# Kernel optimization log

Hardware: AMD Instinct MI355X
Metric: run time of the kernel (lower is better)

Reference implementation:

```python
import jax, jax.numpy as jnp
import numpy as np

N_NODES = 100000
N_EDGES = 3200000
IN_DIM = 256
EMB_DIM = 64
BATCH = 4096
WEIGHT_DECAY = 1e-4


def setup_inputs() -> dict:
    key = jax.random.key(0)
    ks = jax.random.split(key, 8)
    feats = jax.random.normal(ks[0], (N_NODES, IN_DIM), dtype=jnp.float32)
    W = jax.random.normal(ks[1], (IN_DIM, EMB_DIM), dtype=jnp.float32) * (1.0 / np.sqrt(IN_DIM))
    edge_row = jax.random.randint(ks[2], (N_EDGES,), 0, N_NODES, dtype=jnp.int32)
    edge_col = jax.random.randint(ks[3], (N_EDGES,), 0, N_NODES, dtype=jnp.int32)
    edge_val = jax.random.uniform(ks[4], (N_EDGES,), dtype=jnp.float32) * 0.05  # normalized adj weights
    idx1 = jax.random.randint(ks[5], (BATCH,), 0, N_NODES, dtype=jnp.int32)
    idx2 = jax.random.randint(ks[6], (BATCH,), 0, N_NODES, dtype=jnp.int32)
    neg_idx = jax.random.randint(ks[7], (BATCH,), 0, N_NODES, dtype=jnp.int32)
    return {"feats": feats, "W": W, "edge_row": edge_row, "edge_col": edge_col,
            "edge_val": edge_val, "idx1": idx1, "idx2": idx2, "neg_idx": neg_idx}


def reference(feats, W, edge_row, edge_col, edge_val, idx1, idx2, neg_idx):
    # GraphConvolution: tanh( A_sparse @ (X @ W) ), A in COO form
    xw = feats @ W                                              # [N, D]
    msgs = edge_val[:, None] * xw[edge_col]                     # [E, D] gather + scale
    h = jax.ops.segment_sum(msgs, edge_row, num_segments=N_NODES)  # sparse-dense matmul
    h = jnp.tanh(h)
    # tf.nn.l2_normalize(embedding, 1)
    sq = jnp.sum(h * h, axis=1, keepdims=True)
    emb = h * jax.lax.rsqrt(jnp.maximum(sq, 1e-12))             # [N, D]
    # embedding lookups
    o1, o2, on = emb[idx1], emb[idx2], emb[neg_idx]             # [B, D] each
    y_ui = jnp.sum(o1 * o2, axis=1)
    y_uj = jnp.sum(o1 * on, axis=1)
    # BPR loss + weight decay (tf.nn.l2_loss = 0.5*sum(x^2))
    bpr = jnp.sum(-jax.nn.log_sigmoid(y_ui - y_uj))
    loss = (bpr + WEIGHT_DECAY * 0.5 * jnp.sum(emb * emb)) / jnp.float32(BATCH)
    return loss
```

## Files before the change

kernel.cpp:

```cpp
#include <hip/hip_runtime.h>
#include <cmath>

#define N_NODES 100000
#define N_EDGES 3200000
#define IN_DIM 256
#define EMB 64
#define BATCH 4096
#define MWAVES 6250
#define NBUCK 782
#define BROWS 128
#define BSTRIDE 4608
#define EPB 4096

typedef unsigned long long u64;
typedef unsigned int u32;
typedef unsigned short u16;
typedef __attribute__((ext_vector_type(8))) short bf16x8;
typedef __attribute__((ext_vector_type(4))) float f32x4;

__device__ __forceinline__ float wave_sum(float v) {
#pragma unroll
    for (int m = 1; m < 64; m <<= 1) v += __shfl_xor(v, m, 64);
    return v;
}

__device__ __forceinline__ u16 f2bf_rne(float f) {
    u32 u = __float_as_uint(f);
    u32 r = ((u >> 16) & 1u) + 0x7FFFu;
    return (u16)((u + r) >> 16);
}

__device__ __forceinline__ float bf2f(u32 bits16) {
    return __uint_as_float(bits16 << 16);
}

__global__ __launch_bounds__(256) void mfma_gemm_kernel(const float* __restrict__ feats,
                                                        const float* __restrict__ W,
                                                        u16* __restrict__ xwb) {
    __shared__ u16 wlds[32 * 64 * 8];
    const int tid = threadIdx.x;
    for (int idx = tid; idx < 32 * 64; idx += 256) {
        const int f = idx >> 6, lane = idx & 63;
        const int kt = f >> 2, nt = f & 3;
        const int k0 = kt * 32 + (lane >> 4) * 8;
        const int n  = nt * 16 + (lane & 15);
        u32 buf[4];
#pragma unroll
        for (int jj = 0; jj < 4; ++jj) {
            u16 lo = f2bf_rne(W[(size_t)(k0 + 2 * jj) * EMB + n]);
            u16 hi = f2bf_rne(W[(size_t)(k0 + 2 * jj + 1) * EMB + n]);
            buf[jj] = (u32)lo | ((u32)hi << 16);
        }
        *(uint4*)&wlds[idx * 8] = *(uint4*)buf;
    }
    __syncthreads();

    const int wave = tid >> 6, lane = tid & 63;
    const int wid = blockIdx.x * 4 + wave;
    if (wid >= MWAVES) return;
    const int row0 = wid * 16;
    const int arow = row0 + (lane & 15);
    const int kbase = (lane >> 4) * 8;
    const float* fr = feats + (size_t)arow * IN_DIM + kbase;

    float4 av[16];
#pragma unroll
    for (int kt = 0; kt < 8; ++kt) {
        av[2 * kt]     = *(const float4*)(fr + kt * 32);
        av[2 * kt + 1] = *(const float4*)(fr + kt * 32 + 4);
    }

    f32x4 acc[4] = {};
    const u16* wl = &wlds[lane * 8];
#pragma unroll
    for (int kt = 0; kt < 8; ++kt) {
        float4 a0 = av[2 * kt], a1 = av[2 * kt + 1];
        u32 ab[4];
        ab[0] = (u32)f2bf_rne(a0.x) | ((u32)f2bf_rne(a0.y) << 16);
        ab[1] = (u32)f2bf_rne(a0.z) | ((u32)f2bf_rne(a0.w) << 16);
        ab[2] = (u32)f2bf_rne(a1.x) | ((u32)f2bf_rne(a1.y) << 16);
        ab[3] = (u32)f2bf_rne(a1.z) | ((u32)f2bf_rne(a1.w) << 16);
        bf16x8 afrag = *(bf16x8*)ab;
#pragma unroll
        for (int nt = 0; nt < 4; ++nt) {
            bf16x8 bfrag = *(const bf16x8*)&wl[(kt * 4 + nt) * 512];
            acc[nt] = __builtin_amdgcn_mfma_f32_16x16x32_bf16(afrag, bfrag, acc[nt], 0, 0, 0);
        }
    }
    const int rb = row0 + (lane >> 4) * 4;
    const int cb = lane & 15;
#pragma unroll
    for (int nt = 0; nt < 4; ++nt)
#pragma unroll
        for (int r = 0; r < 4; ++r)
            xwb[(size_t)(rb + r) * EMB + nt * 16 + cb] = f2bf_rne(acc[nt][r]);
}

__global__ __launch_bounds__(256) void passA_kernel(const int* __restrict__ erow,
                                                    const int* __restrict__ ecol,
                                                    const float* __restrict__ eval,
                                                    u32* __restrict__ gcursor,
                                                    u64* __restrict__ sorted) {
    __shared__ u64 stage[EPB];
    __shared__ u32 hist[1024];
    __shared__ u32 offs[1024];
    __shared__ u32 cursor[1024];
    __shared__ u32 gbase[1024];
    __shared__ u32 partial[256];

    const int tid = threadIdx.x;
    const int e0 = blockIdx.x * EPB;
    const int total = min(EPB, N_EDGES - e0);

    for (int i = tid; i < 1024; i += 256) hist[i] = 0;
    __syncthreads();

    u64 ent[16];
    int eb[16];
#pragma unroll
    for (int j = 0; j < 16; ++j) {
        const int e = e0 + j * 256 + tid;
        if (e < N_EDGES) {
            const int r = erow[e];
            const int c = ecol[e];
            const u16 vb = f2bf_rne(eval[e]);
            ent[j] = (u64)(u32)r | ((u64)(u32)c << 17) | ((u64)vb << 34);
            eb[j] = r >> 7;
            atomicAdd(&hist[eb[j]], 1u);
        } else {
            eb[j] = -1;
        }
    }
    __syncthreads();

    u32 local[4], s = 0;
#pragma unroll
    for (int q = 0; q < 4; ++q) {
        local[q] = s;
        s += hist[4 * tid + q];
    }
    partial[tid] = s;
    __syncthreads();
    for (int off = 1; off < 256; off <<= 1) {
        u32 x = (tid >= off) ? partial[tid - off] : 0;
        __syncthreads();
        partial[tid] += x;
        __syncthreads();
    }
    const u32 base = partial[tid] - s;
#pragma unroll
    for (int q = 0; q < 4; ++q) {
        offs[4 * tid + q] = base + local[q];
        cursor[4 * tid + q] = base + local[q];
    }
    __syncthreads();

#pragma unroll
    for (int j = 0; j < 16; ++j) {
        if (eb[j] >= 0) {
            u32 pos = atomicAdd(&cursor[eb[j]], 1u);
            stage[pos] = ent[j];
        }
    }
    __syncthreads();

    for (int b = tid; b < 1024; b += 256) {
        const u32 cnt = cursor[b] - offs[b];
        gbase[b] = cnt ? atomicAdd(&gcursor[b], cnt) : 0;
    }
    __syncthreads();

    for (int i = tid; i < total; i += 256) {
        const u64 p = stage[i];
        const int b = (int)(p & 0x1FFFFu) >> 7;
        const u32 gpos = gbase[b] + ((u32)i - offs[b]);
        if (gpos < BSTRIDE) sorted[(size_t)b * BSTRIDE + gpos] = p;
    }
}

__global__ __launch_bounds__(1024, 8) void gather_kernel(const u16* __restrict__ xwb,
                                                         u64* __restrict__ sorted,
                                                         const u32* __restrict__ gcursor,
                                                         float* __restrict__ accumA) {
    __shared__ u64 stage[BSTRIDE];
    __shared__ u32 rhist[BROWS], roff[BROWS], rcur[BROWS], sc[BROWS];
    __shared__ float part[16];
    const int tid = threadIdx.x, wave = tid >> 6, lane = tid & 63;
    const int b = blockIdx.x;
    u64* gbase = sorted + (size_t)b * BSTRIDE;
    const int cnt = min((int)gcursor[b], BSTRIDE);

    if (tid < BROWS) rhist[tid] = 0;
    __syncthreads();

    u64 ent[5];
    int nloc = 0;
    for (int i = tid; i < cnt; i += 1024) {
        u64 p = gbase[i];
        ent[nloc++] = p;
        atomicAdd(&rhist[(int)(p & 127u)], 1u);
    }
    __syncthreads();

    if (tid < BROWS) sc[tid] = rhist[tid];
    __syncthreads();
    for (int off = 1; off < BROWS; off <<= 1) {
        u32 x = (tid < BROWS && tid >= off) ? sc[tid - off] : 0;
        __syncthreads();
        if (tid < BROWS) sc[tid] += x;
        __syncthreads();
    }
    if (tid < BROWS) {
        roff[tid] = sc[tid] - rhist[tid];
        rcur[tid] = sc[tid] - rhist[tid];
    }
    __syncthreads();

    for (int j = 0; j < nloc; ++j) {
        const u64 p = ent[j];
        const u32 pos = atomicAdd(&rcur[(int)(p & 127u)], 1u);
        stage[pos] = p;
    }
    __syncthreads();

    u16* embp = (u16*)gbase;
    float wd = 0.f;
    for (int rr = 0; rr < 8; ++rr) {
        const int r = wave * 8 + rr;
        const int s0 = roff[r], n = rhist[r];
        float acc = 0.f;
        int j = s0;
        const int e2 = s0 + n;
        for (; j + 7 < e2; j += 8) {
            u64 p0 = stage[j],     p1 = stage[j + 1], p2 = stage[j + 2], p3 = stage[j + 3];
            u64 p4 = stage[j + 4], p5 = stage[j + 5], p6 = stage[j + 6], p7 = stage[j + 7];
            float x0 = bf2f(xwb[(size_t)((p0 >> 17) & 0x1FFFFu) * EMB + lane]);
            float x1 = bf2f(xwb[(size_t)((p1 >> 17) & 0x1FFFFu) * EMB + lane]);
            float x2 = bf2f(xwb[(size_t)((p2 >> 17) & 0x1FFFFu) * EMB + lane]);
            float x3 = bf2f(xwb[(size_t)((p3 >> 17) & 0x1FFFFu) * EMB + lane]);
            float x4 = bf2f(xwb[(size_t)((p4 >> 17) & 0x1FFFFu) * EMB + lane]);
            float x5 = bf2f(xwb[(size_t)((p5 >> 17) & 0x1FFFFu) * EMB + lane]);
            float x6 = bf2f(xwb[(size_t)((p6 >> 17) & 0x1FFFFu) * EMB + lane]);
            float x7 = bf2f(xwb[(size_t)((p7 >> 17) & 0x1FFFFu) * EMB + lane]);
            acc += bf2f((u32)(p0 >> 34) & 0xFFFFu) * x0 + bf2f((u32)(p1 >> 34) & 0xFFFFu) * x1;
            acc += bf2f((u32)(p2 >> 34) & 0xFFFFu) * x2 + bf2f((u32)(p3 >> 34) & 0xFFFFu) * x3;
            acc += bf2f((u32)(p4 >> 34) & 0xFFFFu) * x4 + bf2f((u32)(p5 >> 34) & 0xFFFFu) * x5;
            acc += bf2f((u32)(p6 >> 34) & 0xFFFFu) * x6 + bf2f((u32)(p7 >> 34) & 0xFFFFu) * x7;
        }
        for (; j < e2; ++j) {
            u64 p = stage[j];
            acc += bf2f((u32)(p >> 34) & 0xFFFFu) * bf2f(xwb[(size_t)((p >> 17) & 0x1FFFFu) * EMB + lane]);
        }
        float x = tanhf(acc);
        float sq = wave_sum(x * x);
        if (b * BROWS + r < N_NODES)
            embp[r * EMB + lane] = f2bf_rne(x * rsqrtf(fmaxf(sq, 1e-12f)));
        wd += sq / fmaxf(sq, 1e-12f);
    }
    if (lane == 0) part[wave] = wd;
    __syncthreads();
    if (tid == 0) {
        float v = 0.f;
#pragma unroll
        for (int w = 0; w < 16; ++w) v += part[w];
        unsafeAtomicAdd(&accumA[b & 255], v);
    }
}

__device__ __forceinline__ float emb_ld(const u64* __restrict__ sorted, int row, int lane) {
    const u16* rp = (const u16*)(sorted + (size_t)(row >> 7) * BSTRIDE) + (row & 127) * EMB;
    return bf2f(rp[lane]);
}

__global__ __launch_bounds__(256) void bpr_kernel(const u64* __restrict__ sorted,
                                                  const int* __restrict__ idx1,
                                                  const int* __restrict__ idx2,
                                                  const int* __restrict__ nidx,
                                                  float* __restrict__ accumB) {
    const int wave = threadIdx.x >> 6, lane = threadIdx.x & 63;
    const int i = blockIdx.x * 4 + wave;
    float o1 = emb_ld(sorted, idx1[i], lane);
    float o2 = emb_ld(sorted, idx2[i], lane);
    float on = emb_ld(sorted, nidx[i], lane);
    float yui = wave_sum(o1 * o2);
    float yuj = wave_sum(o1 * on);
    if (lane == 0) {
        float x = yui - yuj;
        float li = (x > 0.f) ? log1pf(expf(-x)) : (-x + log1pf(expf(x)));
        unsafeAtomicAdd(&accumB[i & 255], li);
    }
}

__global__ __launch_bounds__(64) void finalize_kernel(const float* __restrict__ accumA,
                                                      const float* __restrict__ accumB,
                                                      float* __restrict__ out) {
    const int t = threadIdx.x;
    float wd = 0.f, bp = 0.f;
#pragma unroll
    for (int k = 0; k < 4; ++k) {
        wd += accumA[t + 64 * k];
        bp += accumB[t + 64 * k];
    }
    wd = wave_sum(wd);
    bp = wave_sum(bp);
    if (t == 0) out[0] = (bp + 1e-4f * 0.5f * wd) / (float)BATCH;
}

extern "C" void kernel_launch(void* const* d_in, const int* in_sizes, int n_in,
                              void* d_out, int out_size, void* d_ws, size_t ws_size,
                              hipStream_t stream) {
    const float* feats = (const float*)d_in[0];
    const float* W     = (const float*)d_in[1];
    const int*   erow  = (const int*)d_in[2];
    const int*   ecol  = (const int*)d_in[3];
    const float* eval  = (const float*)d_in[4];
    const int*   idx1  = (const int*)d_in[5];
    const int*   idx2  = (const int*)d_in[6];
    const int*   nidx  = (const int*)d_in[7];
    float* out = (float*)d_out;

    u16*   xwb     = (u16*)d_ws;
    u64*   sorted  = (u64*)(xwb + (size_t)N_NODES * EMB);
    u32*   gcursor = (u32*)(sorted + (size_t)NBUCK * BSTRIDE);
    float* accumA  = (float*)(gcursor + 1024);
    float* accumB  = accumA + 256;

    hipMemsetAsync(gcursor, 0, (1024 + 512) * sizeof(u32), stream);

    mfma_gemm_kernel<<<(MWAVES + 3) / 4, 256, 0, stream>>>(feats, W, xwb);
    passA_kernel<<<(N_EDGES + EPB - 1) / EPB, 256, 0, stream>>>(erow, ecol, eval, gcursor, sorted);
    gather_kernel<<<NBUCK, 1024, 0, stream>>>(xwb, sorted, gcursor, accumA);
    bpr_kernel<<<BATCH / 4, 256, 0, stream>>>(sorted, idx1, idx2, nidx, accumB);
    finalize_kernel<<<1, 64, 0, stream>>>(accumA, accumB, out);
}
```

Baseline: 345.3 us.

## Fuse GEMM and edge bucketing into one kernel, fold finalize into BPR

Merges the bf16 MFMA projection GEMM and the edge-bucketing pass into a single launch with interleaved block types, so the compute-bound GEMM and the memory-bound scatter can run at the same time. Block size moves to 512 and the GEMM loads its A operand in two halves to cut register pressure. Gather blocks shrink to 512 threads, each wave now handling 16 rows. The finalize kernel is removed: the last BPR block, found with an atomic counter, does the final reduction, which saves a launch but adds a threadfence and an atomic per block.

```diff
diff --git a/kernel.cpp b/kernel.cpp
--- a/kernel.cpp
+++ b/kernel.cpp
@@ -11,6 +11,8 @@
 #define BROWS 128
 #define BSTRIDE 4608
 #define EPB 4096
+#define GSUB 782
+#define ASUB 782
 
 typedef unsigned long long u64;
 typedef unsigned int u32;
@@ -34,157 +36,157 @@
     return __uint_as_float(bits16 << 16);
 }
 
-__global__ __launch_bounds__(256) void mfma_gemm_kernel(const float* __restrict__ feats,
-                                                        const float* __restrict__ W,
-                                                        u16* __restrict__ xwb) {
-    __shared__ u16 wlds[32 * 64 * 8];
+__global__ __launch_bounds__(512, 6) void fused_kernel(const float* __restrict__ feats,
+                                                       const float* __restrict__ W,
+                                                       u16* __restrict__ xwb,
+                                                       const int* __restrict__ erow,
+                                                       const int* __restrict__ ecol,
+                                                       const float* __restrict__ eval,
+                                                       u32* __restrict__ gcursor,
+                                                       u64* __restrict__ sorted) {
+    __shared__ u64 smem[5376];
     const int tid = threadIdx.x;
-    for (int idx = tid; idx < 32 * 64; idx += 256) {
-        const int f = idx >> 6, lane = idx & 63;
-        const int kt = f >> 2, nt = f & 3;
-        const int k0 = kt * 32 + (lane >> 4) * 8;
-        const int n  = nt * 16 + (lane & 15);
-        u32 buf[4];
-#pragma unroll
-        for (int jj = 0; jj < 4; ++jj) {
-            u16 lo = f2bf_rne(W[(size_t)(k0 + 2 * jj) * EMB + n]);
-            u16 hi = f2bf_rne(W[(size_t)(k0 + 2 * jj + 1) * EMB + n]);
-            buf[jj] = (u32)lo | ((u32)hi << 16);
-        }
-        *(uint4*)&wlds[idx * 8] = *(uint4*)buf;
-    }
-    __syncthreads();
-
-    const int wave = tid >> 6, lane = tid & 63;
-    const int wid = blockIdx.x * 4 + wave;
-    if (wid >= MWAVES) return;
-    const int row0 = wid * 16;
-    const int arow = row0 + (lane & 15);
-    const int kbase = (lane >> 4) * 8;
-    const float* fr = feats + (size_t)arow * IN_DIM + kbase;
-
-    float4 av[16];
-#pragma unroll
-    for (int kt = 0; kt < 8; ++kt) {
-        av[2 * kt]     = *(const float4*)(fr + kt * 32);
-        av[2 * kt + 1] = *(const float4*)(fr + kt * 32 + 4);
-    }
-
-    f32x4 acc[4] = {};
-    const u16* wl = &wlds[lane * 8];
-#pragma unroll
-    for (int kt = 0; kt < 8; ++kt) {
-        float4 a0 = av[2 * kt], a1 = av[2 * kt + 1];
-        u32 ab[4];
-        ab[0] = (u32)f2bf_rne(a0.x) | ((u32)f2bf_rne(a0.y) << 16);
-        ab[1] = (u32)f2bf_rne(a0.z) | ((u32)f2bf_rne(a0.w) << 16);
-        ab[2] = (u32)f2bf_rne(a1.x) | ((u32)f2bf_rne(a1.y) << 16);
-        ab[3] = (u32)f2bf_rne(a1.z) | ((u32)f2bf_rne(a1.w) << 16);
-        bf16x8 afrag = *(bf16x8*)ab;
-#pragma unroll
-        for (int nt = 0; nt < 4; ++nt) {
-            bf16x8 bfrag = *(const bf16x8*)&wl[(kt * 4 + nt) * 512];
-            acc[nt] = __builtin_amdgcn_mfma_f32_16x16x32_bf16(afrag, bfrag, acc[nt], 0, 0, 0);
-        }
-    }
-    const int rb = row0 + (lane >> 4) * 4;
-    const int cb = lane & 15;
-#pragma unroll
-    for (int nt = 0; nt < 4; ++nt)
-#pragma unroll
-        for (int r = 0; r < 4; ++r)
-            xwb[(size_t)(rb + r) * EMB + nt * 16 + cb] = f2bf_rne(acc[nt][r]);
-}
-
-__global__ __launch_bounds__(256) void passA_kernel(const int* __restrict__ erow,
-                                                    const int* __restrict__ ecol,
-                                                    const float* __restrict__ eval,
-                                                    u32* __restrict__ gcursor,
-                                                    u64* __restrict__ sorted) {
-    __shared__ u64 stage[EPB];
-    __shared__ u32 hist[1024];
-    __shared__ u32 offs[1024];
-    __shared__ u32 cursor[1024];
-    __shared__ u32 gbase[1024];
-    __shared__ u32 partial[256];
-
-    const int tid = threadIdx.x;
-    const int e0 = blockIdx.x * EPB;
-    const int total = min(EPB, N_EDGES - e0);
-
-    for (int i = tid; i < 1024; i += 256) hist[i] = 0;
-    __syncthreads();
-
-    u64 ent[16];
-    int eb[16];
-#pragma unroll
-    for (int j = 0; j < 16; ++j) {
-        const int e = e0 + j * 256 + tid;
-        if (e < N_EDGES) {
-            const int r = erow[e];
-            const int c = ecol[e];
-            const u16 vb = f2bf_rne(eval[e]);
-            ent[j] = (u64)(u32)r | ((u64)(u32)c << 17) | ((u64)vb << 34);
-            eb[j] = r >> 7;
-            atomicAdd(&hist[eb[j]], 1u);
-        } else {
-            eb[j] = -1;
-        }
-    }
-    __syncthreads();
-
-    u32 local[4], s = 0;
-#pragma unroll
-    for (int q = 0; q < 4; ++q) {
-        local[q] = s;
-        s += hist[4 * tid + q];
-    }
-    partial[tid] = s;
-    __syncthreads();
-    for (int off = 1; off < 256; off <<= 1) {
-        u32 x = (tid >= off) ? partial[tid - off] : 0;
-        __syncthreads();
-        partial[tid] += x;
-        __syncthreads();
-    }
-    const u32 base = partial[tid] - s;
-#pragma unroll
-    for (int q = 0; q < 4; ++q) {
-        offs[4 * tid + q] = base + local[q];
-        cursor[4 * tid + q] = base + local[q];
-    }
-    __syncthreads();
-
-#pragma unroll
-    for (int j = 0; j < 16; ++j) {
-        if (eb[j] >= 0) {
-            u32 pos = atomicAdd(&cursor[eb[j]], 1u);
-            stage[pos] = ent[j];
-        }
-    }
-    __syncthreads();
-
-    for (int b = tid; b < 1024; b += 256) {
-        const u32 cnt = cursor[b] - offs[b];
-        gbase[b] = cnt ? atomicAdd(&gcursor[b], cnt) : 0;
-    }
-    __syncthreads();
-
-    for (int i = tid; i < total; i += 256) {
-        const u64 p = stage[i];
-        const int b = (int)(p & 0x1FFFFu) >> 7;
-        const u32 gpos = gbase[b] + ((u32)i - offs[b]);
-        if (gpos < BSTRIDE) sorted[(size_t)b * BSTRIDE + gpos] = p;
-    }
-}
-
-__global__ __launch_bounds__(1024, 8) void gather_kernel(const u16* __restrict__ xwb,
-                                                         u64* __restrict__ sorted,
-                                                         const u32* __restrict__ gcursor,
-                                                         float* __restrict__ accumA) {
+    const int type = blockIdx.x & 1;
+    const int sub = blockIdx.x >> 1;
+
+    if (type == 0) {
+        u16* wlds = (u16*)smem;
+        for (int idx = tid; idx < 32 * 64; idx += 512) {
+            const int f = idx >> 6, lane = idx & 63;
+            const int kt = f >> 2, nt = f & 3;
+            const int k0 = kt * 32 + (lane >> 4) * 8;
+            const int n  = nt * 16 + (lane & 15);
+            u32 buf[4];
+#pragma unroll
+            for (int jj = 0; jj < 4; ++jj) {
+                u16 lo = f2bf_rne(W[(size_t)(k0 + 2 * jj) * EMB + n]);
+                u16 hi = f2bf_rne(W[(size_t)(k0 + 2 * jj + 1) * EMB + n]);
+                buf[jj] = (u32)lo | ((u32)hi << 16);
+            }
+            *(uint4*)&wlds[idx * 8] = *(uint4*)buf;
+        }
+        __syncthreads();
+
+        const int wave = tid >> 6, lane = tid & 63;
+        const int wid = sub * 8 + wave;
+        if (wid >= MWAVES) return;
+        const int row0 = wid * 16;
+        const int arow = row0 + (lane & 15);
+        const int kbase = (lane >> 4) * 8;
+        const float* fr = feats + (size_t)arow * IN_DIM + kbase;
+
+        f32x4 acc[4] = {};
+        const u16* wl = &wlds[lane * 8];
+#pragma unroll
+        for (int half = 0; half < 2; ++half) {
+            float4 av[8];
+#pragma unroll
+            for (int k2 = 0; k2 < 4; ++k2) {
+                const int kt = half * 4 + k2;
+                av[2 * k2]     = *(const float4*)(fr + kt * 32);
+                av[2 * k2 + 1] = *(const float4*)(fr + kt * 32 + 4);
+            }
+#pragma unroll
+            for (int k2 = 0; k2 < 4; ++k2) {
+                const int kt = half * 4 + k2;
+                float4 a0 = av[2 * k2], a1 = av[2 * k2 + 1];
+                u32 ab[4];
+                ab[0] = (u32)f2bf_rne(a0.x) | ((u32)f2bf_rne(a0.y) << 16);
+                ab[1] = (u32)f2bf_rne(a0.z) | ((u32)f2bf_rne(a0.w) << 16);
+                ab[2] = (u32)f2bf_rne(a1.x) | ((u32)f2bf_rne(a1.y) << 16);
+                ab[3] = (u32)f2bf_rne(a1.z) | ((u32)f2bf_rne(a1.w) << 16);
+                bf16x8 afrag = *(bf16x8*)ab;
+#pragma unroll
+                for (int nt = 0; nt < 4; ++nt) {
+                    bf16x8 bfrag = *(const bf16x8*)&wl[(kt * 4 + nt) * 512];
+                    acc[nt] = __builtin_amdgcn_mfma_f32_16x16x32_bf16(afrag, bfrag, acc[nt], 0, 0, 0);
+                }
+            }
+        }
+        const int rb = row0 + (lane >> 4) * 4;
+        const int cb = lane & 15;
+#pragma unroll
+        for (int nt = 0; nt < 4; ++nt)
+#pragma unroll
+            for (int r = 0; r < 4; ++r)
+                xwb[(size_t)(rb + r) * EMB + nt * 16 + cb] = f2bf_rne(acc[nt][r]);
+    } else {
+        u64* stage    = smem;
+        u32* histoffs = (u32*)(smem + 4096);
+        u32* cursor   = (u32*)(smem + 4608);
+        u32* partial  = (u32*)(smem + 5120);
+
+        const int e0 = sub * EPB;
+        const int total = min(EPB, N_EDGES - e0);
+
+        for (int i = tid; i < 1024; i += 512) histoffs[i] = 0;
+        __syncthreads();
+
+        u64 ent[8];
+        int eb[8];
+#pragma unroll
+        for (int j = 0; j < 8; ++j) {
+            const int e = e0 + j * 512 + tid;
+            if (e < N_EDGES) {
+                const int r = erow[e];
+                const int c = ecol[e];
+                const u16 vb = f2bf_rne(eval[e]);
+                ent[j] = (u64)(u32)r | ((u64)(u32)c << 17) | ((u64)vb << 34);
+                eb[j] = r >> 7;
+                atomicAdd(&histoffs[eb[j]], 1u);
+            } else {
+                eb[j] = -1;
+            }
+        }
+        __syncthreads();
+
+        const u32 c0 = histoffs[2 * tid], c1 = histoffs[2 * tid + 1];
+        const u32 s = c0 + c1;
+        partial[tid] = s;
+        __syncthreads();
+        for (int off = 1; off < 512; off <<= 1) {
+            u32 x = (tid >= off) ? partial[tid - off] : 0;
+            __syncthreads();
+            partial[tid] += x;
+            __syncthreads();
+        }
+        const u32 base = partial[tid] - s;
+        histoffs[2 * tid] = base;       cursor[2 * tid] = base;
+        histoffs[2 * tid + 1] = base + c0; cursor[2 * tid + 1] = base + c0;
+        __syncthreads();
+
+#pragma unroll
+        for (int j = 0; j < 8; ++j) {
+            if (eb[j] >= 0) {
+                u32 pos = atomicAdd(&cursor[eb[j]], 1u);
+                stage[pos] = ent[j];
+            }
+        }
+        __syncthreads();
+
+        for (int b = tid; b < 1024; b += 512) {
+            const u32 cnt = cursor[b] - histoffs[b];
+            const u32 gb = cnt ? atomicAdd(&gcursor[b], cnt) : 0;
+            cursor[b] = gb - histoffs[b];
+        }
+        __syncthreads();
+
+        for (int i = tid; i < total; i += 512) {
+            const u64 p = stage[i];
+            const int b = (int)(p & 0x1FFFFu) >> 7;
+            const u32 gpos = cursor[b] + (u32)i;
+            if (gpos < BSTRIDE) sorted[(size_t)b * BSTRIDE + gpos] = p;
+        }
+    }
+}
+
+__global__ __launch_bounds__(512, 8) void gather_kernel(const u16* __restrict__ xwb,
+                                                        u64* __restrict__ sorted,
+                                                        const u32* __restrict__ gcursor,
+                                                        float* __restrict__ accumA) {
     __shared__ u64 stage[BSTRIDE];
     __shared__ u32 rhist[BROWS], roff[BROWS], rcur[BROWS], sc[BROWS];
-    __shared__ float part[16];
+    __shared__ float part[8];
     const int tid = threadIdx.x, wave = tid >> 6, lane = tid & 63;
     const int b = blockIdx.x;
     u64* gbase = sorted + (size_t)b * BSTRIDE;
@@ -193,9 +195,9 @@
     if (tid < BROWS) rhist[tid] = 0;
     __syncthreads();
 
-    u64 ent[5];
+    u64 ent[9];
     int nloc = 0;
-    for (int i = tid; i < cnt; i += 1024) {
+    for (int i = tid; i < cnt; i += 512) {
         u64 p = gbase[i];
         ent[nloc++] = p;
         atomicAdd(&rhist[(int)(p & 127u)], 1u);
@@ -225,8 +227,8 @@
 
     u16* embp = (u16*)gbase;
     float wd = 0.f;
-    for (int rr = 0; rr < 8; ++rr) {
-        const int r = wave * 8 + rr;
+    for (int rr = 0; rr < 16; ++rr) {
+        const int r = wave * 16 + rr;
         const int s0 = roff[r], n = rhist[r];
         float acc = 0.f;
         int j = s0;
@@ -262,7 +264,7 @@
     if (tid == 0) {
         float v = 0.f;
 #pragma unroll
-        for (int w = 0; w < 16; ++w) v += part[w];
+        for (int w = 0; w < 8; ++w) v += part[w];
         unsafeAtomicAdd(&accumA[b & 255], v);
     }
 }
@@ -276,8 +278,13 @@
                                                   const int* __restrict__ idx1,
                                                   const int* __restrict__ idx2,
                                                   const int* __restrict__ nidx,
-                                                  float* __restrict__ accumB) {
-    const int wave = threadIdx.x >> 6, lane = threadIdx.x & 63;
+                                                  float* __restrict__ accumA,
+                                                  float* __restrict__ accumB,
+                                                  u32* __restrict__ done,
+                                                  float* __restrict__ out) {
+    __shared__ int lastflag;
+    const int tid = threadIdx.x;
+    const int wave = tid >> 6, lane = tid & 63;
     const int i = blockIdx.x * 4 + wave;
     float o1 = emb_ld(sorted, idx1[i], lane);
     float o2 = emb_ld(sorted, idx2[i], lane);
@@ -289,21 +296,21 @@
         float li = (x > 0.f) ? log1pf(expf(-x)) : (-x + log1pf(expf(x)));
         unsafeAtomicAdd(&accumB[i & 255], li);
     }
-}
-
-__global__ __launch_bounds__(64) void finalize_kernel(const float* __restrict__ accumA,
-                                                      const float* __restrict__ accumB,
-                                                      float* __restrict__ out) {
-    const int t = threadIdx.x;
-    float wd = 0.f, bp = 0.f;
-#pragma unroll
-    for (int k = 0; k < 4; ++k) {
-        wd += accumA[t + 64 * k];
-        bp += accumB[t + 64 * k];
-    }
-    wd = wave_sum(wd);
-    bp = wave_sum(bp);
-    if (t == 0) out[0] = (bp + 1e-4f * 0.5f * wd) / (float)BATCH;
+    __threadfence();
+    __syncthreads();
+    if (tid == 0) lastflag = (atomicAdd(done, 1u) == (u32)(gridDim.x - 1)) ? 1 : 0;
+    __syncthreads();
+    if (lastflag && tid < 64) {
+        float wd = 0.f, bp = 0.f;
+#pragma unroll
+        for (int k = 0; k < 4; ++k) {
+            wd += accumA[tid + 64 * k];
+            bp += accumB[tid + 64 * k];
+        }
+        wd = wave_sum(wd);
+        bp = wave_sum(bp);
+        if (tid == 0) out[0] = (bp + 1e-4f * 0.5f * wd) / (float)BATCH;
+    }
 }
 
 extern "C" void kernel_launch(void* const* d_in, const int* in_sizes, int n_in,
@@ -324,12 +331,11 @@
     u32*   gcursor = (u32*)(sorted + (size_t)NBUCK * BSTRIDE);
     float* accumA  = (float*)(gcursor + 1024);
     float* accumB  = accumA + 256;
-
-    hipMemsetAsync(gcursor, 0, (1024 + 512) * sizeof(u32), stream);
-
-    mfma_gemm_kernel<<<(MWAVES + 3) / 4, 256, 0, stream>>>(feats, W, xwb);
-    passA_kernel<<<(N_EDGES + EPB - 1) / EPB, 256, 0, stream>>>(erow, ecol, eval, gcursor, sorted);
-    gather_kernel<<<NBUCK, 1024, 0, stream>>>(xwb, sorted, gcursor, accumA);
-    bpr_kernel<<<BATCH / 4, 256, 0, stream>>>(sorted, idx1, idx2, nidx, accumB);
-    finalize_kernel<<<1, 64, 0, stream>>>(accumA, accumB, out);
-}
+    u32*   done    = (u32*)(accumB + 256);
+
+    hipMemsetAsync(gcursor, 0, (1024 + 256 + 256 + 16) * sizeof(u32), stream);
+
+    fused_kernel<<<GSUB + ASUB, 512, 0, stream>>>(feats, W, xwb, erow, ecol, eval, gcursor, sorted);
+    gather_kernel<<<NBUCK, 512, 0, stream>>>(xwb, sorted, gcursor, accumA);
+    bpr_kernel<<<BATCH / 4, 256, 0, stream>>>(sorted, idx1, idx2, nidx, accumA, accumB, done, out);
+}
```

Result: slower. 373.3 us (+8.1%).
